# Performance work log

Measured on AMD Instinct MI355X. Metric: run time of the kernel, lower is better.

## Reference

```python
import jax, jax.numpy as jnp
import numpy as np


def bin_op_s(a, b, w):
    """Differentiable weighted sum over the 16 real-valued binary logic gates.
    a, b: [B, O] soft-boolean inputs; w: [O, 16] gate mixture weights.
    Gate order matches difflogic's bin_op_s.
    """
    ab = a * b
    a_plus_b = a + b
    one = jnp.asarray(1.0, a.dtype)
    # w[:, i] broadcasts [O] against [B, O]
    return (
        # w[:, 0] * 0 (FALSE) contributes nothing
        w[:, 1] * ab                              # a AND b
        + w[:, 2] * (a - ab)                      # a AND NOT b
        + w[:, 3] * a                             # a
        + w[:, 4] * (b - ab)                      # NOT a AND b
        + w[:, 5] * b                             # b
        + w[:, 6] * (a_plus_b - 2.0 * ab)         # a XOR b
        + w[:, 7] * (a_plus_b - ab)               # a OR b
        + w[:, 8] * (one - (a_plus_b - ab))       # NOR
        + w[:, 9] * (one - (a_plus_b - 2.0 * ab)) # XNOR
        + w[:, 10] * (one - b)                    # NOT b
        + w[:, 11] * (one - b + ab)               # b -> a
        + w[:, 12] * (one - a)                    # NOT a
        + w[:, 13] * (one - a + ab)               # a -> b
        + w[:, 14] * (one - ab)                   # NAND
        + w[:, 15] * one                          # TRUE
    )


def setup_inputs() -> dict:
    key = jax.random.key(0)
    k_x, k_w, k_a, k_b = jax.random.split(key, 4)
    B, IN_DIM, OUT_DIM = 2048, 8192, 16384
    x = jax.random.uniform(k_x, (B, IN_DIM), dtype=jnp.float32)
    weights = jax.random.normal(k_w, (OUT_DIM, 16), dtype=jnp.float32)
    idx_a = jax.random.randint(k_a, (OUT_DIM,), 0, IN_DIM, dtype=jnp.int64 if jax.config.jax_enable_x64 else jnp.int32)
    idx_b = jax.random.randint(k_b, (OUT_DIM,), 0, IN_DIM, dtype=jnp.int64 if jax.config.jax_enable_x64 else jnp.int32)
    return {"x": x, "weights": weights, "idx_a": idx_a, "idx_b": idx_b}


def reference(x, weights, idx_a, idx_b):
    # training-mode forward_python: gather the two connected inputs per neuron,
    # softmax the 16 gate logits, and take the soft gate mixture.
    a = x[:, idx_a]  # [B, out_dim]
    b = x[:, idx_b]  # [B, out_dim]
    w = jax.nn.softmax(weights, axis=-1)  # [out_dim, 16]
    return bin_op_s(a, b, w)
```

## Files before the change

### kernel.cpp

```cpp
#include <hip/hip_runtime.h>


#define THREADS 256
#define ROWS 2
#define IN_DIM_C 8192

__global__ __launch_bounds__(THREADS) void coeffs_k(
    const float* __restrict__ w,
    float* __restrict__ c0o, float* __restrict__ cao,
    float* __restrict__ cbo, float* __restrict__ cabo,
    int OUT_DIM)
{
    const int j = blockIdx.x * THREADS + threadIdx.x;
    if (j >= OUT_DIM) return;

    float wv[16];
    const float4* wp = reinterpret_cast<const float4*>(w + (size_t)j * 16);
    #pragma unroll
    for (int q = 0; q < 4; ++q) {
        float4 v = wp[q];
        wv[q * 4 + 0] = v.x; wv[q * 4 + 1] = v.y;
        wv[q * 4 + 2] = v.z; wv[q * 4 + 3] = v.w;
    }

    float m = -1e30f;
    #pragma unroll
    for (int g = 0; g < 16; ++g) m = fmaxf(m, wv[g]);

    float e[16]; float s = 0.f;
    #pragma unroll
    for (int g = 0; g < 16; ++g) { e[g] = __expf(wv[g] - m); s += e[g]; }
    const float inv = 1.f / s;

    const float C0  = e[8] + e[9] + e[10] + e[11] + e[12] + e[13] + e[14] + e[15];
    const float Ca  = e[2] + e[3] + e[6] + e[7] - e[8] - e[9] - e[12] - e[13];
    const float Cb  = e[4] + e[5] + e[6] + e[7] - e[8] - e[9] - e[10] - e[11];
    const float Cab = e[1] - e[2] - e[4] - 2.f * e[6] - e[7]
                    + e[8] + 2.f * e[9] + e[11] + e[13] - e[14];

    c0o[j]  = C0  * inv;
    cao[j]  = Ca  * inv;
    cbo[j]  = Cb  * inv;
    cabo[j] = Cab * inv;
}

__global__ __launch_bounds__(THREADS) void row_k(
    const float* __restrict__ x,
    const float4* __restrict__ c04, const float4* __restrict__ ca4,
    const float4* __restrict__ cb4, const float4* __restrict__ cab4,
    const int4* __restrict__ ia4,
    const int4* __restrict__ ib4,
    float4* __restrict__ out4,
    int IN_DIM, int OUT_DIM)
{
    __shared__ float sx[ROWS * IN_DIM_C];

    const int row0 = blockIdx.x * ROWS;
    const int tid  = threadIdx.x;
    const int nchunk = OUT_DIM / (THREADS * 4);

    int4   va = ia4[tid];
    int4   vb = ib4[tid];
    float4 f0 = c04[tid], fa = ca4[tid], fb = cb4[tid], fc = cab4[tid];

    {
        const float4* xr4 = reinterpret_cast<const float4*>(x + (size_t)row0 * IN_DIM);
        float4* s4 = reinterpret_cast<float4*>(sx);
        const int n4 = ROWS * IN_DIM / 4;
        #pragma unroll
        for (int t = tid; t < n4; t += THREADS) s4[t] = xr4[t];
    }
    __syncthreads();

    const int o4 = OUT_DIM / 4;
    float4* __restrict__ orow0 = out4 + (size_t)row0 * o4;
    float4* __restrict__ orow1 = orow0 + o4;

    #pragma unroll 1
    for (int c = 0; c < nchunk; ++c) {
        const int4   cva = va, cvb = vb;
        const float4 g0 = f0, ga = fa, gb = fb, gc = fc;
        const int j4 = c * THREADS + tid;

        if (c + 1 < nchunk) {
            const int nj4 = j4 + THREADS;
            va = ia4[nj4]; vb = ib4[nj4];
            f0 = c04[nj4]; fa = ca4[nj4]; fb = cb4[nj4]; fc = cab4[nj4];
        }

        float4 r0, r1;
        {
            const float a0 = sx[cva.x], b0 = sx[cvb.x];
            const float a1 = sx[cva.y], b1 = sx[cvb.y];
            const float a2 = sx[cva.z], b2 = sx[cvb.z];
            const float a3 = sx[cva.w], b3 = sx[cvb.w];
            r0.x = fmaf(a0 * b0, gc.x, fmaf(b0, gb.x, fmaf(a0, ga.x, g0.x)));
            r0.y = fmaf(a1 * b1, gc.y, fmaf(b1, gb.y, fmaf(a1, ga.y, g0.y)));
            r0.z = fmaf(a2 * b2, gc.z, fmaf(b2, gb.z, fmaf(a2, ga.z, g0.z)));
            r0.w = fmaf(a3 * b3, gc.w, fmaf(b3, gb.w, fmaf(a3, ga.w, g0.w)));
        }
        {
            const float a0 = sx[IN_DIM_C + cva.x], b0 = sx[IN_DIM_C + cvb.x];
            const float a1 = sx[IN_DIM_C + cva.y], b1 = sx[IN_DIM_C + cvb.y];
            const float a2 = sx[IN_DIM_C + cva.z], b2 = sx[IN_DIM_C + cvb.z];
            const float a3 = sx[IN_DIM_C + cva.w], b3 = sx[IN_DIM_C + cvb.w];
            r1.x = fmaf(a0 * b0, gc.x, fmaf(b0, gb.x, fmaf(a0, ga.x, g0.x)));
            r1.y = fmaf(a1 * b1, gc.y, fmaf(b1, gb.y, fmaf(a1, ga.y, g0.y)));
            r1.z = fmaf(a2 * b2, gc.z, fmaf(b2, gb.z, fmaf(a2, ga.z, g0.z)));
            r1.w = fmaf(a3 * b3, gc.w, fmaf(b3, gb.w, fmaf(a3, ga.w, g0.w)));
        }
        orow0[j4] = r0;
        orow1[j4] = r1;
    }
}

extern "C" void kernel_launch(void* const* d_in, const int* in_sizes, int n_in,
                              void* d_out, int out_size, void* d_ws, size_t ws_size,
                              hipStream_t stream) {
    const float* x     = (const float*)d_in[0];
    const float* w     = (const float*)d_in[1];
    const int*   idx_a = (const int*)d_in[2];
    const int*   idx_b = (const int*)d_in[3];
    float*       out   = (float*)d_out;

    const int OUT_DIM = in_sizes[2];
    const int B       = out_size / OUT_DIM;
    const int IN_DIM  = in_sizes[0] / B;

    float* c0  = (float*)d_ws;
    float* ca  = c0 + OUT_DIM;
    float* cb  = ca + OUT_DIM;
    float* cab = cb + OUT_DIM;

    coeffs_k<<<(OUT_DIM + THREADS - 1) / THREADS, THREADS, 0, stream>>>(
        w, c0, ca, cb, cab, OUT_DIM);

    row_k<<<B / ROWS, THREADS, 0, stream>>>(
        x,
        reinterpret_cast<const float4*>(c0),
        reinterpret_cast<const float4*>(ca),
        reinterpret_cast<const float4*>(cb),
        reinterpret_cast<const float4*>(cab),
        reinterpret_cast<const int4*>(idx_a),
        reinterpret_cast<const int4*>(idx_b),
        reinterpret_cast<float4*>(out),
        IN_DIM, OUT_DIM);
}
```

Before: 201.5 us.

## Interleave two rows in LDS as float2, use nontemporal stores, 512 threads

The shared-memory copy of the two batch rows is interleaved into float2 pairs, so each gathered index costs one 64-bit LDS read instead of two 32-bit reads. Output stores become nontemporal so the large streamed output does not pollute cache. The row kernel block size rises to 512 threads, halving the chunk count per thread. The interleaving adds shuffling work during the staging load, and the larger block may change occupancy.

Measured after the change: 193.4 us. 4.0% less time.

```diff
diff --git a/kernel.cpp b/kernel.cpp
--- a/kernel.cpp
+++ b/kernel.cpp
@@ -1,17 +1,20 @@
 #include <hip/hip_runtime.h>
 
 
-#define THREADS 256
+#define THREADS 512
+#define CTHREADS 256
 #define ROWS 2
 #define IN_DIM_C 8192
 
-__global__ __launch_bounds__(THREADS) void coeffs_k(
+typedef float floatx4 __attribute__((ext_vector_type(4)));
+
+__global__ __launch_bounds__(CTHREADS) void coeffs_k(
     const float* __restrict__ w,
     float* __restrict__ c0o, float* __restrict__ cao,
     float* __restrict__ cbo, float* __restrict__ cabo,
     int OUT_DIM)
 {
-    const int j = blockIdx.x * THREADS + threadIdx.x;
+    const int j = blockIdx.x * CTHREADS + threadIdx.x;
     if (j >= OUT_DIM) return;
 
     float wv[16];
@@ -50,10 +53,10 @@
     const float4* __restrict__ cb4, const float4* __restrict__ cab4,
     const int4* __restrict__ ia4,
     const int4* __restrict__ ib4,
-    float4* __restrict__ out4,
+    float* __restrict__ out,
     int IN_DIM, int OUT_DIM)
 {
-    __shared__ float sx[ROWS * IN_DIM_C];
+    __shared__ float2 sx2[IN_DIM_C];
 
     const int row0 = blockIdx.x * ROWS;
     const int tid  = threadIdx.x;
@@ -64,17 +67,24 @@
     float4 f0 = c04[tid], fa = ca4[tid], fb = cb4[tid], fc = cab4[tid];
 
     {
-        const float4* xr4 = reinterpret_cast<const float4*>(x + (size_t)row0 * IN_DIM);
-        float4* s4 = reinterpret_cast<float4*>(sx);
-        const int n4 = ROWS * IN_DIM / 4;
+        const float4* xr0 = reinterpret_cast<const float4*>(x + (size_t)row0 * IN_DIM);
+        const float4* xr1 = reinterpret_cast<const float4*>(x + (size_t)(row0 + 1) * IN_DIM);
+        float4* s4 = reinterpret_cast<float4*>(sx2);
+        const int n4 = IN_DIM / 4;
         #pragma unroll
-        for (int t = tid; t < n4; t += THREADS) s4[t] = xr4[t];
+        for (int t = tid; t < n4; t += THREADS) {
+            const float4 r0 = xr0[t];
+            const float4 r1 = xr1[t];
+            s4[2 * t + 0] = make_float4(r0.x, r1.x, r0.y, r1.y);
+            s4[2 * t + 1] = make_float4(r0.z, r1.z, r0.w, r1.w);
+        }
     }
     __syncthreads();
 
-    const int o4 = OUT_DIM / 4;
-    float4* __restrict__ orow0 = out4 + (size_t)row0 * o4;
-    float4* __restrict__ orow1 = orow0 + o4;
+    floatx4* __restrict__ orow0 =
+        reinterpret_cast<floatx4*>(out + (size_t)row0 * OUT_DIM);
+    floatx4* __restrict__ orow1 =
+        reinterpret_cast<floatx4*>(out + (size_t)(row0 + 1) * OUT_DIM);
 
     #pragma unroll 1
     for (int c = 0; c < nchunk; ++c) {
@@ -88,29 +98,24 @@
             f0 = c04[nj4]; fa = ca4[nj4]; fb = cb4[nj4]; fc = cab4[nj4];
         }
 
-        float4 r0, r1;
-        {
-            const float a0 = sx[cva.x], b0 = sx[cvb.x];
-            const float a1 = sx[cva.y], b1 = sx[cvb.y];
-            const float a2 = sx[cva.z], b2 = sx[cvb.z];
-            const float a3 = sx[cva.w], b3 = sx[cvb.w];
-            r0.x = fmaf(a0 * b0, gc.x, fmaf(b0, gb.x, fmaf(a0, ga.x, g0.x)));
-            r0.y = fmaf(a1 * b1, gc.y, fmaf(b1, gb.y, fmaf(a1, ga.y, g0.y)));
-            r0.z = fmaf(a2 * b2, gc.z, fmaf(b2, gb.z, fmaf(a2, ga.z, g0.z)));
-            r0.w = fmaf(a3 * b3, gc.w, fmaf(b3, gb.w, fmaf(a3, ga.w, g0.w)));
-        }
-        {
-            const float a0 = sx[IN_DIM_C + cva.x], b0 = sx[IN_DIM_C + cvb.x];
-            const float a1 = sx[IN_DIM_C + cva.y], b1 = sx[IN_DIM_C + cvb.y];
-            const float a2 = sx[IN_DIM_C + cva.z], b2 = sx[IN_DIM_C + cvb.z];
-            const float a3 = sx[IN_DIM_C + cva.w], b3 = sx[IN_DIM_C + cvb.w];
-            r1.x = fmaf(a0 * b0, gc.x, fmaf(b0, gb.x, fmaf(a0, ga.x, g0.x)));
-            r1.y = fmaf(a1 * b1, gc.y, fmaf(b1, gb.y, fmaf(a1, ga.y, g0.y)));
-            r1.z = fmaf(a2 * b2, gc.z, fmaf(b2, gb.z, fmaf(a2, ga.z, g0.z)));
-            r1.w = fmaf(a3 * b3, gc.w, fmaf(b3, gb.w, fmaf(a3, ga.w, g0.w)));
-        }
-        orow0[j4] = r0;
-        orow1[j4] = r1;
+        const float2 a0 = sx2[cva.x], b0 = sx2[cvb.x];
+        const float2 a1 = sx2[cva.y], b1 = sx2[cvb.y];
+        const float2 a2 = sx2[cva.z], b2 = sx2[cvb.z];
+        const float2 a3 = sx2[cva.w], b3 = sx2[cvb.w];
+
+        floatx4 r0, r1;
+        r0.x = fmaf(a0.x * b0.x, gc.x, fmaf(b0.x, gb.x, fmaf(a0.x, ga.x, g0.x)));
+        r0.y = fmaf(a1.x * b1.x, gc.y, fmaf(b1.x, gb.y, fmaf(a1.x, ga.y, g0.y)));
+        r0.z = fmaf(a2.x * b2.x, gc.z, fmaf(b2.x, gb.z, fmaf(a2.x, ga.z, g0.z)));
+        r0.w = fmaf(a3.x * b3.x, gc.w, fmaf(b3.x, gb.w, fmaf(a3.x, ga.w, g0.w)));
+
+        r1.x = fmaf(a0.y * b0.y, gc.x, fmaf(b0.y, gb.x, fmaf(a0.y, ga.x, g0.x)));
+        r1.y = fmaf(a1.y * b1.y, gc.y, fmaf(b1.y, gb.y, fmaf(a1.y, ga.y, g0.y)));
+        r1.z = fmaf(a2.y * b2.y, gc.z, fmaf(b2.y, gb.z, fmaf(a2.y, ga.z, g0.z)));
+        r1.w = fmaf(a3.y * b3.y, gc.w, fmaf(b3.y, gb.w, fmaf(a3.y, ga.w, g0.w)));
+
+        __builtin_nontemporal_store(r0, &orow0[j4]);
+        __builtin_nontemporal_store(r1, &orow1[j4]);
     }
 }
 
@@ -132,7 +137,7 @@
     float* cb  = ca + OUT_DIM;
     float* cab = cb + OUT_DIM;
 
-    coeffs_k<<<(OUT_DIM + THREADS - 1) / THREADS, THREADS, 0, stream>>>(
+    coeffs_k<<<(OUT_DIM + CTHREADS - 1) / CTHREADS, CTHREADS, 0, stream>>>(
         w, c0, ca, cb, cab, OUT_DIM);
 
     row_k<<<B / ROWS, THREADS, 0, stream>>>(
@@ -143,6 +148,6 @@
         reinterpret_cast<const float4*>(cab),
         reinterpret_cast<const int4*>(idx_a),
         reinterpret_cast<const int4*>(idx_b),
-        reinterpret_cast<float4*>(out),
+        out,
         IN_DIM, OUT_DIM);
 }
```
